# Optimization experiments

Hardware: AMD Instinct MI355X
Metric: run time of the kernel (lower is better)

The kernel has to match this reference:

```python
import jax, jax.numpy as jnp
import numpy as np

N_NODES = 100000
NEG_SLOPE = 0.01  # F.leaky_relu default


def _hetero_graphconv(x, src, dst, W, b, n_nodes):
    """HeteroGraphConv(aggregate='sum') of DGL GraphConv(norm='both') per edge type.

    x: [N, d_in]; src/dst: [R, E] int; W: [R, d_in, d_out]; b: [R, d_out].
    """
    n_rel = W.shape[0]
    ones = None
    out = jnp.zeros((n_nodes, W.shape[2]), dtype=x.dtype)
    for r in range(n_rel):  # small fixed number of relations
        s, d = src[r], dst[r]
        e_ones = jnp.ones(s.shape, dtype=x.dtype)
        deg_out = jnp.clip(jax.ops.segment_sum(e_ones, s, num_segments=n_nodes), 1.0)
        deg_in = jnp.clip(jax.ops.segment_sum(e_ones, d, num_segments=n_nodes), 1.0)
        # norm='both': scale src by out_deg^-1/2, aggregate, scale dst by in_deg^-1/2.
        # Apply weight before gather (aggregation is linear) to shrink edge traffic.
        h = (x * (deg_out ** -0.5)[:, None]) @ W[r]          # [N, d_out]
        agg = jax.ops.segment_sum(h[s], d, num_segments=n_nodes)  # gather-scatter over edges
        out = out + agg * (deg_in ** -0.5)[:, None] + b[r]
    return out


def setup_inputs() -> dict:
    key = jax.random.key(0)
    ks = jax.random.split(key, 8)
    d_in, d_h, d_out, n_cls, n_rel, n_edges = 256, 128, 128, 16, 3, 600000
    x = jax.random.normal(ks[0], (N_NODES, d_in), dtype=jnp.float32)
    src = jax.random.randint(ks[1], (n_rel, n_edges), 0, N_NODES, dtype=jnp.int32)
    dst = jax.random.randint(ks[2], (n_rel, n_edges), 0, N_NODES, dtype=jnp.int32)
    W0 = jax.random.normal(ks[3], (n_rel, d_in, d_h), dtype=jnp.float32) * (d_in ** -0.5)
    b0 = jnp.zeros((n_rel, d_h), dtype=jnp.float32)
    W1 = jax.random.normal(ks[4], (n_rel, d_h, d_out), dtype=jnp.float32) * (d_h ** -0.5)
    b1 = jnp.zeros((n_rel, d_out), dtype=jnp.float32)
    fc_W = jax.random.normal(ks[5], (d_out, n_cls), dtype=jnp.float32) * (d_out ** -0.5)
    fc_b = jnp.zeros((n_cls,), dtype=jnp.float32)
    return {"x": x, "src": src, "dst": dst, "W0": W0, "b0": b0,
            "W1": W1, "b1": b1, "fc_W": fc_W, "fc_b": fc_b}


def reference(x, src, dst, W0, b0, W1, b1, fc_W, fc_b):
    n = x.shape[0]
    h = _hetero_graphconv(x, src, dst, W0, b0, n)
    h = jax.nn.leaky_relu(h, negative_slope=NEG_SLOPE)  # dropout rate 0 (eval)
    h = _hetero_graphconv(h, src, dst, W1, b1, n)       # last layer: no activation
    logits = h @ fc_W + fc_b
    return (h, logits)
```

## Files before the change

### kernel.cpp

```cpp
#include <hip/hip_runtime.h>
#include <hip/hip_bf16.h>
#include <stdint.h>


typedef __attribute__((ext_vector_type(8))) short bf16x8;
typedef __attribute__((ext_vector_type(4))) float f32x4;
typedef unsigned short u16;

#define SCAN_T 256
#define SCAN_E 8
#define SCAN_BLK (SCAN_T * SCAN_E)

__global__ __launch_bounds__(256)
void hist_kernel(const int* __restrict__ src, const int* __restrict__ dst,
                 int* __restrict__ cnt_out8, int* __restrict__ cnt_in8,
                 int E, int N) {
    int e = blockIdx.x * blockDim.x + threadIdx.x;
    int r = blockIdx.y;
    if (e >= E) return;
    int copy = blockIdx.x & 7;
    size_t base = ((size_t)copy * 3 + r) * N;
    atomicAdd(cnt_out8 + base + src[(size_t)r * E + e], 1);
    atomicAdd(cnt_in8  + base + dst[(size_t)r * E + e], 1);
}

__global__ __launch_bounds__(256)
void reduce_scales_kernel(const int* __restrict__ cnt_out8, const int* __restrict__ cnt_in8,
                          float* __restrict__ s_out, float* __restrict__ s_in,
                          int* __restrict__ cnt_in, int total ) {
    int i = blockIdx.x * blockDim.x + threadIdx.x;
    if (i >= total) return;
    int co = 0, ci = 0;
#pragma unroll
    for (int c = 0; c < 8; c++) {
        co += cnt_out8[(size_t)c * total + i];
        ci += cnt_in8[(size_t)c * total + i];
    }
    s_out[i] = rsqrtf(fmaxf((float)co, 1.0f));
    s_in[i]  = rsqrtf(fmaxf((float)ci, 1.0f));
    cnt_in[i] = ci;
}

__global__ __launch_bounds__(SCAN_T)
void scan1_kernel(const int* __restrict__ cnt, int* __restrict__ pre,
                  int* __restrict__ bsums, int N) {
    int r = blockIdx.y, b = blockIdx.x, t = threadIdx.x;
    int base = b * SCAN_BLK + t * SCAN_E;
    int v[SCAN_E], s = 0;
#pragma unroll
    for (int j = 0; j < SCAN_E; j++) {
        int idx = base + j;
        v[j] = (idx < N) ? cnt[(size_t)r * N + idx] : 0;
        s += v[j];
    }
    __shared__ int sd[SCAN_T];
    sd[t] = s;
    __syncthreads();
    for (int off = 1; off < SCAN_T; off <<= 1) {
        int x = (t >= off) ? sd[t - off] : 0;
        __syncthreads();
        sd[t] += x;
        __syncthreads();
    }
    if (t == SCAN_T - 1) bsums[r * gridDim.x + b] = sd[t];
    int run = sd[t] - s;
#pragma unroll
    for (int j = 0; j < SCAN_E; j++) {
        int idx = base + j;
        if (idx < N) pre[(size_t)r * (N + 1) + idx] = run;
        run += v[j];
    }
}

__global__ void scan2_kernel(int* __restrict__ bsums, int* __restrict__ row_start,
                             int nb, int N) {
    for (int r = 0; r < 3; r++) {
        int run = 0;
        for (int b = 0; b < nb; b++) {
            int t = bsums[r * nb + b];
            bsums[r * nb + b] = run;
            run += t;
        }
        row_start[(size_t)r * (N + 1) + N] = run;
    }
}

__global__ __launch_bounds__(SCAN_T)
void scan3_kernel(int* __restrict__ pre, const int* __restrict__ bsums,
                  int* __restrict__ cursor, int nb, int N) {
    int r = blockIdx.y, b = blockIdx.x, t = threadIdx.x;
    int add = bsums[r * nb + b];
    int base = b * SCAN_BLK + t * SCAN_E;
#pragma unroll
    for (int j = 0; j < SCAN_E; j++) {
        int idx = base + j;
        if (idx < N) {
            int val = pre[(size_t)r * (N + 1) + idx] + add;
            pre[(size_t)r * (N + 1) + idx] = val;
            cursor[(size_t)r * N + idx] = val;
        }
    }
}

__global__ __launch_bounds__(256)
void bucket_fill_kernel(const int* __restrict__ src, const int* __restrict__ dst,
                        int* __restrict__ cursor, int* __restrict__ esrc,
                        int E, int N) {
    int e = blockIdx.x * blockDim.x + threadIdx.x;
    int r = blockIdx.y;
    if (e >= E) return;
    int d = dst[(size_t)r * E + e];
    int pos = atomicAdd(cursor + (size_t)r * N + d, 1);
    esrc[(size_t)r * E + pos] = src[(size_t)r * E + e];
}

__global__ __launch_bounds__(256)
void prep_w_kernel(const float* __restrict__ W0, const float* __restrict__ W1,
                   u16* __restrict__ w0hi, u16* __restrict__ w0lo,
                   u16* __restrict__ w1hi, u16* __restrict__ w1lo) {
    int idx = blockIdx.x * blockDim.x + threadIdx.x;
    const int n0 = 3 * 256 * 128;
    const int n1 = 3 * 128 * 128;
    if (idx >= n0 + n1) return;
    float f;
    u16 *phi, *plo;
    int oidx;
    if (idx < n0) {
        int r = idx / 32768, rem = idx % 32768;
        int n = rem / 256, k = rem % 256;
        f = W0[(size_t)r * 32768 + (size_t)k * 128 + n];
        phi = w0hi; plo = w0lo; oidx = idx;
    } else {
        int i2 = idx - n0;
        int r = i2 / 16384, rem = i2 % 16384;
        int n = rem / 128, k = rem % 128;
        f = W1[(size_t)r * 16384 + (size_t)k * 128 + n];
        phi = w1hi; plo = w1lo; oidx = i2;
    }
    uint32_t u = __float_as_uint(f);
    phi[oidx] = (u16)(u >> 16);
    float lo = f - __uint_as_float(u & 0xFFFF0000u);
    uint32_t ul = __float_as_uint(lo);
    plo[oidx] = (u16)((ul + 0x7FFFu + ((ul >> 16) & 1u)) >> 16);
}

__global__ __launch_bounds__(256)
void gemm_split_bf16(const float* __restrict__ A, const float* __restrict__ s_out,
                     const u16* __restrict__ Whi_all, const u16* __restrict__ Wlo_all,
                     u16* __restrict__ Cout_all, int M, int K, int Nn) {
    const int r = blockIdx.y;
    const float* scale = s_out + (size_t)r * Nn;
    const u16* Whi = Whi_all + (size_t)r * K * 128;
    const u16* Wlo = Wlo_all + (size_t)r * K * 128;
    u16* Cout = Cout_all + (size_t)r * Nn * 128;

    __shared__ u16 As_hi[128][40];
    __shared__ u16 As_lo[128][40];
    __shared__ u16 Bs_hi[128][40];
    __shared__ u16 Bs_lo[128][40];

    const int tid  = threadIdx.x;
    const int m0   = blockIdx.x * 128;
    const int lane = tid & 63;
    const int wave = tid >> 6;
    const int wm   = (wave & 1) * 64;
    const int wn   = (wave >> 1) * 64;
    const int lm   = lane & 15;
    const int kq   = (lane >> 4) * 8;

    f32x4 acc[4][4];
#pragma unroll
    for (int i = 0; i < 4; i++)
#pragma unroll
        for (int j = 0; j < 4; j++) acc[i][j] = (f32x4){0.f, 0.f, 0.f, 0.f};

    const int srow = tid >> 1;
    const int skb  = (tid & 1) * 16;

    const bool valid = (m0 + srow) < M;
    const float sval = valid ? scale[m0 + srow] : 0.f;
    const float* arow = A + (size_t)(m0 + srow) * K;
    const u16* whrow = Whi + (size_t)srow * K;
    const u16* wlrow = Wlo + (size_t)srow * K;

    for (int k0 = 0; k0 < K; k0 += 32) {
        float fa[16];
        if (valid) {
            *(float4*)&fa[0]  = *(const float4*)(arow + k0 + skb);
            *(float4*)&fa[4]  = *(const float4*)(arow + k0 + skb + 4);
            *(float4*)&fa[8]  = *(const float4*)(arow + k0 + skb + 8);
            *(float4*)&fa[12] = *(const float4*)(arow + k0 + skb + 12);
        } else {
#pragma unroll
            for (int i = 0; i < 16; i++) fa[i] = 0.f;
        }
        uint32_t ah[8], al[8];
#pragma unroll
        for (int p = 0; p < 8; p++) {
            float f0 = fa[2 * p] * sval, f1 = fa[2 * p + 1] * sval;
            uint32_t u0 = __float_as_uint(f0), u1 = __float_as_uint(f1);
            ah[p] = (u0 >> 16) | (u1 & 0xFFFF0000u);
            float l0 = f0 - __uint_as_float(u0 & 0xFFFF0000u);
            float l1 = f1 - __uint_as_float(u1 & 0xFFFF0000u);
            al[p] = (__float_as_uint(l0) >> 16) | (__float_as_uint(l1) & 0xFFFF0000u);
        }
        *(uint4*)&As_hi[srow][skb]     = *(uint4*)&ah[0];
        *(uint4*)&As_hi[srow][skb + 8] = *(uint4*)&ah[4];
        *(uint4*)&As_lo[srow][skb]     = *(uint4*)&al[0];
        *(uint4*)&As_lo[srow][skb + 8] = *(uint4*)&al[4];

        *(uint4*)&Bs_hi[srow][skb]     = *(const uint4*)(whrow + k0 + skb);
        *(uint4*)&Bs_hi[srow][skb + 8] = *(const uint4*)(whrow + k0 + skb + 8);
        *(uint4*)&Bs_lo[srow][skb]     = *(const uint4*)(wlrow + k0 + skb);
        *(uint4*)&Bs_lo[srow][skb + 8] = *(const uint4*)(wlrow + k0 + skb + 8);

        __syncthreads();

        bf16x8 a_hi[4], a_lo[4], b_hi[4], b_lo[4];
#pragma unroll
        for (int i = 0; i < 4; i++) {
            a_hi[i] = *(const bf16x8*)&As_hi[wm + i * 16 + lm][kq];
            a_lo[i] = *(const bf16x8*)&As_lo[wm + i * 16 + lm][kq];
            b_hi[i] = *(const bf16x8*)&Bs_hi[wn + i * 16 + lm][kq];
            b_lo[i] = *(const bf16x8*)&Bs_lo[wn + i * 16 + lm][kq];
        }
#pragma unroll
        for (int i = 0; i < 4; i++)
#pragma unroll
            for (int j = 0; j < 4; j++) {
                acc[i][j] = __builtin_amdgcn_mfma_f32_16x16x32_bf16(a_hi[i], b_hi[j], acc[i][j], 0, 0, 0);
                acc[i][j] = __builtin_amdgcn_mfma_f32_16x16x32_bf16(a_lo[i], b_hi[j], acc[i][j], 0, 0, 0);
                acc[i][j] = __builtin_amdgcn_mfma_f32_16x16x32_bf16(a_hi[i], b_lo[j], acc[i][j], 0, 0, 0);
            }
        __syncthreads();
    }

    const int rq = (lane >> 4) * 4;
#pragma unroll
    for (int i = 0; i < 4; i++) {
        int mbase = m0 + wm + i * 16 + rq;
#pragma unroll
        for (int j = 0; j < 4; j++) {
            int col = wn + j * 16 + lm;
#pragma unroll
            for (int rg = 0; rg < 4; rg++) {
                int m = mbase + rg;
                if (m < M) {
                    uint32_t u = __float_as_uint(acc[i][j][rg]);
                    Cout[(size_t)m * 128 + col] =
                        (u16)((u + 0x7FFFu + ((u >> 16) & 1u)) >> 16);
                }
            }
        }
    }
}

#define BF16_LO(u) __uint_as_float((u) << 16)
#define BF16_HI(u) __uint_as_float((u) & 0xFFFF0000u)

__device__ __forceinline__ void gather_rel(const uint32_t* __restrict__ h,
                                           const int* __restrict__ es,
                                           int beg, int end,
                                           float& ox, float& oy, float w) {
    float ax = 0.f, ay = 0.f, cx = 0.f, cy = 0.f;
    int e = beg;
    for (; e + 4 <= end; e += 4) {
        int s0 = es[e], s1 = es[e + 1], s2 = es[e + 2], s3 = es[e + 3];
        uint32_t u0 = h[(size_t)s0 * 64];
        uint32_t u1 = h[(size_t)s1 * 64];
        uint32_t u2 = h[(size_t)s2 * 64];
        uint32_t u3 = h[(size_t)s3 * 64];
        ax += BF16_LO(u0); ay += BF16_HI(u0);
        cx += BF16_LO(u1); cy += BF16_HI(u1);
        ax += BF16_LO(u2); ay += BF16_HI(u2);
        cx += BF16_LO(u3); cy += BF16_HI(u3);
    }
    if (e + 2 <= end) {
        int s0 = es[e], s1 = es[e + 1];
        uint32_t u0 = h[(size_t)s0 * 64];
        uint32_t u1 = h[(size_t)s1 * 64];
        ax += BF16_LO(u0); ay += BF16_HI(u0);
        cx += BF16_LO(u1); cy += BF16_HI(u1);
        e += 2;
    }
    if (e < end) {
        uint32_t u0 = h[(size_t)es[e] * 64];
        ax += BF16_LO(u0); ay += BF16_HI(u0);
    }
    ox += (ax + cx) * w;
    oy += (ay + cy) * w;
}

__global__ __launch_bounds__(256)
void gather_l0(const u16* __restrict__ hb, const int* __restrict__ row_start,
               const int* __restrict__ esrc, const float* __restrict__ s_in,
               const float* __restrict__ b, float* __restrict__ out, int N, int E) {
    int node = blockIdx.x * 4 + (threadIdx.x >> 6);
    if (node >= N) return;
    int lane = threadIdx.x & 63;
    float tx = 0.f, ty = 0.f;
#pragma unroll
    for (int r = 0; r < 3; r++) {
        const int* rs = row_start + (size_t)r * (N + 1);
        gather_rel((const uint32_t*)hb + (size_t)r * N * 64 + lane,
                   esrc + (size_t)r * E, rs[node], rs[node + 1],
                   tx, ty, s_in[(size_t)r * N + node]);
    }
    int c0 = lane * 2;
    tx += b[c0] + b[128 + c0] + b[256 + c0];
    ty += b[c0 + 1] + b[128 + c0 + 1] + b[256 + c0 + 1];
    tx = fmaxf(tx, 0.f) + 0.01f * fminf(tx, 0.f);
    ty = fmaxf(ty, 0.f) + 0.01f * fminf(ty, 0.f);
    *(float2*)(out + (size_t)node * 128 + c0) = make_float2(tx, ty);
}

__global__ __launch_bounds__(256)
void gather_l1(const u16* __restrict__ hb, const int* __restrict__ row_start,
               const int* __restrict__ esrc, const float* __restrict__ s_in,
               const float* __restrict__ b, const float* __restrict__ fcW,
               const float* __restrict__ fcb, float* __restrict__ out_h,
               float* __restrict__ out_logits, int N, int E) {
    int node = blockIdx.x * 4 + (threadIdx.x >> 6);
    if (node >= N) return;
    int lane = threadIdx.x & 63;
    float tx = 0.f, ty = 0.f;
#pragma unroll
    for (int r = 0; r < 3; r++) {
        const int* rs = row_start + (size_t)r * (N + 1);
        gather_rel((const uint32_t*)hb + (size_t)r * N * 64 + lane,
                   esrc + (size_t)r * E, rs[node], rs[node + 1],
                   tx, ty, s_in[(size_t)r * N + node]);
    }
    int c0 = lane * 2;
    tx += b[c0] + b[128 + c0] + b[256 + c0];
    ty += b[c0 + 1] + b[128 + c0 + 1] + b[256 + c0 + 1];
    *(float2*)(out_h + (size_t)node * 128 + c0) = make_float2(tx, ty);

    const float* fc0 = fcW + (size_t)c0 * 16;
    float p[16];
#pragma unroll
    for (int j = 0; j < 16; j++) p[j] = tx * fc0[j] + ty * fc0[16 + j];
#pragma unroll
    for (int off = 1; off < 64; off <<= 1) {
#pragma unroll
        for (int j = 0; j < 16; j++) p[j] += __shfl_xor(p[j], off);
    }
    if (lane == 0) {
        float* lp = out_logits + (size_t)node * 16;
        *(float4*)(lp + 0)  = make_float4(p[0] + fcb[0],  p[1] + fcb[1],  p[2] + fcb[2],  p[3] + fcb[3]);
        *(float4*)(lp + 4)  = make_float4(p[4] + fcb[4],  p[5] + fcb[5],  p[6] + fcb[6],  p[7] + fcb[7]);
        *(float4*)(lp + 8)  = make_float4(p[8] + fcb[8],  p[9] + fcb[9],  p[10] + fcb[10], p[11] + fcb[11]);
        *(float4*)(lp + 12) = make_float4(p[12] + fcb[12], p[13] + fcb[13], p[14] + fcb[14], p[15] + fcb[15]);
    }
}

extern "C" void kernel_launch(void* const* d_in, const int* in_sizes, int n_in,
                              void* d_out, int out_size, void* d_ws, size_t ws_size,
                              hipStream_t stream) {
    const float* x   = (const float*)d_in[0];
    const int*   src = (const int*)d_in[1];
    const int*   dst = (const int*)d_in[2];
    const float* W0  = (const float*)d_in[3];
    const float* b0  = (const float*)d_in[4];
    const float* W1  = (const float*)d_in[5];
    const float* b1  = (const float*)d_in[6];
    const float* fcW = (const float*)d_in[7];
    const float* fcb = (const float*)d_in[8];

    const int N = in_sizes[0] / 256;
    const int E = in_sizes[1] / 3;
    const int nb = (N + SCAN_BLK - 1) / SCAN_BLK;

    float* out_h      = (float*)d_out;
    float* out_logits = out_h + (size_t)N * 128;

    char* p = (char*)d_ws;
    auto alloc = [&](size_t bytes) -> char* {
        char* q = p;
        p += (bytes + 255) & ~(size_t)255;
        return q;
    };
    float* s_out     = (float*)alloc(3 * (size_t)N * 4);
    float* s_in      = (float*)alloc(3 * (size_t)N * 4);
    int*   cnt8      = (int*)alloc(2 * 8 * 3 * (size_t)N * 4);
    int*   cnt_out8  = cnt8;
    int*   cnt_in8   = cnt8 + 8 * 3 * (size_t)N;
    int*   cnt_in    = (int*)alloc(3 * (size_t)N * 4);
    int*   row_start = (int*)alloc(3 * (size_t)(N + 1) * 4);
    int*   cursor    = (int*)alloc(3 * (size_t)N * 4);
    int*   bsums     = (int*)alloc(1024 * 4);
    int*   esrc      = (int*)alloc(3 * (size_t)E * 4);
    u16*   w0hi      = (u16*)alloc(3 * 256 * 128 * 2);
    u16*   w0lo      = (u16*)alloc(3 * 256 * 128 * 2);
    u16*   w1hi      = (u16*)alloc(3 * 128 * 128 * 2);
    u16*   w1lo      = (u16*)alloc(3 * 128 * 128 * 2);
    u16*   hb        = (u16*)alloc(3 * (size_t)N * 128 * 2);
    float* acc0      = (float*)alloc((size_t)N * 128 * 4);

    hipMemsetAsync(cnt8, 0, 2 * 8 * 3 * (size_t)N * sizeof(int), stream);

    hist_kernel<<<dim3((E + 255) / 256, 3), 256, 0, stream>>>(src, dst, cnt_out8, cnt_in8, E, N);
    reduce_scales_kernel<<<(3 * N + 255) / 256, 256, 0, stream>>>(
        cnt_out8, cnt_in8, s_out, s_in, cnt_in, 3 * N);

    scan1_kernel<<<dim3(nb, 3), SCAN_T, 0, stream>>>(cnt_in, row_start, bsums, N);
    scan2_kernel<<<1, 1, 0, stream>>>(bsums, row_start, nb, N);
    scan3_kernel<<<dim3(nb, 3), SCAN_T, 0, stream>>>(row_start, bsums, cursor, nb, N);
    bucket_fill_kernel<<<dim3((E + 255) / 256, 3), 256, 0, stream>>>(src, dst, cursor, esrc, E, N);

    prep_w_kernel<<<(3 * 256 * 128 + 3 * 128 * 128 + 255) / 256, 256, 0, stream>>>(
        W0, W1, w0hi, w0lo, w1hi, w1lo);

    int gemm_blocks   = (N + 127) / 128;
    int gather_blocks = (N + 3) / 4;

    gemm_split_bf16<<<dim3(gemm_blocks, 3), 256, 0, stream>>>(
        x, s_out, w0hi, w0lo, hb, N, 256, N);
    gather_l0<<<gather_blocks, 256, 0, stream>>>(hb, row_start, esrc, s_in, b0, acc0, N, E);

    gemm_split_bf16<<<dim3(gemm_blocks, 3), 256, 0, stream>>>(
        acc0, s_out, w1hi, w1lo, hb, N, 128, N);
    gather_l1<<<gather_blocks, 256, 0, stream>>>(hb, row_start, esrc, s_in, b1, fcW, fcb,
                                                 out_h, out_logits, N, E);
}
```

Before: 846.3 us.

## Gather edges with 16-byte loads across four edge groups per wave

The gather kernels change from one 4-byte load per lane per edge to a layout where each wave splits into 4 groups of 16 lanes. Each lane loads a uint4 (8 bf16 channels), so four edges are processed in parallel, and the groups are reduced with shuffles. The fc logits reduction is restructured to match, cutting the shuffle work from 16 values over 6 steps to 4 values over 4 steps. The GEMM now applies the per-row src-degree scale in the epilogue instead of on the A input, which changes rounding slightly. Loop iterations past the end of a node's edges are masked, adding some wasted loads when degrees are small.

```diff
diff --git a/kernel.cpp b/kernel.cpp
--- a/kernel.cpp
+++ b/kernel.cpp
@@ -178,7 +178,6 @@
     const int skb  = (tid & 1) * 16;
 
     const bool valid = (m0 + srow) < M;
-    const float sval = valid ? scale[m0 + srow] : 0.f;
     const float* arow = A + (size_t)(m0 + srow) * K;
     const u16* whrow = Whi + (size_t)srow * K;
     const u16* wlrow = Wlo + (size_t)srow * K;
@@ -197,7 +196,7 @@
         uint32_t ah[8], al[8];
 #pragma unroll
         for (int p = 0; p < 8; p++) {
-            float f0 = fa[2 * p] * sval, f1 = fa[2 * p + 1] * sval;
+            float f0 = fa[2 * p], f1 = fa[2 * p + 1];
             uint32_t u0 = __float_as_uint(f0), u1 = __float_as_uint(f1);
             ah[p] = (u0 >> 16) | (u1 & 0xFFFF0000u);
             float l0 = f0 - __uint_as_float(u0 & 0xFFFF0000u);
@@ -240,13 +239,14 @@
     for (int i = 0; i < 4; i++) {
         int mbase = m0 + wm + i * 16 + rq;
 #pragma unroll
-        for (int j = 0; j < 4; j++) {
-            int col = wn + j * 16 + lm;
-#pragma unroll
-            for (int rg = 0; rg < 4; rg++) {
-                int m = mbase + rg;
-                if (m < M) {
-                    uint32_t u = __float_as_uint(acc[i][j][rg]);
+        for (int rg = 0; rg < 4; rg++) {
+            int m = mbase + rg;
+            if (m < M) {
+                float s = scale[m];
+#pragma unroll
+                for (int j = 0; j < 4; j++) {
+                    int col = wn + j * 16 + lm;
+                    uint32_t u = __float_as_uint(acc[i][j][rg] * s);
                     Cout[(size_t)m * 128 + col] =
                         (u16)((u + 0x7FFFu + ((u >> 16) & 1u)) >> 16);
                 }
@@ -258,37 +258,51 @@
 #define BF16_LO(u) __uint_as_float((u) << 16)
 #define BF16_HI(u) __uint_as_float((u) & 0xFFFF0000u)
 
-__device__ __forceinline__ void gather_rel(const uint32_t* __restrict__ h,
-                                           const int* __restrict__ es,
-                                           int beg, int end,
-                                           float& ox, float& oy, float w) {
-    float ax = 0.f, ay = 0.f, cx = 0.f, cy = 0.f;
-    int e = beg;
-    for (; e + 4 <= end; e += 4) {
-        int s0 = es[e], s1 = es[e + 1], s2 = es[e + 2], s3 = es[e + 3];
-        uint32_t u0 = h[(size_t)s0 * 64];
-        uint32_t u1 = h[(size_t)s1 * 64];
-        uint32_t u2 = h[(size_t)s2 * 64];
-        uint32_t u3 = h[(size_t)s3 * 64];
-        ax += BF16_LO(u0); ay += BF16_HI(u0);
-        cx += BF16_LO(u1); cy += BF16_HI(u1);
-        ax += BF16_LO(u2); ay += BF16_HI(u2);
-        cx += BF16_LO(u3); cy += BF16_HI(u3);
-    }
-    if (e + 2 <= end) {
-        int s0 = es[e], s1 = es[e + 1];
-        uint32_t u0 = h[(size_t)s0 * 64];
-        uint32_t u1 = h[(size_t)s1 * 64];
-        ax += BF16_LO(u0); ay += BF16_HI(u0);
-        cx += BF16_LO(u1); cy += BF16_HI(u1);
-        e += 2;
-    }
-    if (e < end) {
-        uint32_t u0 = h[(size_t)es[e] * 64];
-        ax += BF16_LO(u0); ay += BF16_HI(u0);
-    }
-    ox += (ax + cx) * w;
-    oy += (ay + cy) * w;
+#define ADD8(a, u)                                   \
+    do {                                             \
+        a[0] += BF16_LO((u).x); a[1] += BF16_HI((u).x); \
+        a[2] += BF16_LO((u).y); a[3] += BF16_HI((u).y); \
+        a[4] += BF16_LO((u).z); a[5] += BF16_HI((u).z); \
+        a[6] += BF16_LO((u).w); a[7] += BF16_HI((u).w); \
+    } while (0)
+
+__device__ __forceinline__ void gather3(const u16* __restrict__ hb,
+                                        const int* __restrict__ row_start,
+                                        const int* __restrict__ esrc,
+                                        const float* __restrict__ s_in,
+                                        int node, int g, int c, int N, int E,
+                                        float* __restrict__ tot ) {
+    const uint4* hbase = (const uint4*)hb;
+#pragma unroll
+    for (int r = 0; r < 3; r++) {
+        const int* rs = row_start + (size_t)r * (N + 1);
+        const int* es = esrc + (size_t)r * E;
+        const uint4* h = hbase + (size_t)r * N * 16 + c;
+        int beg = rs[node], end = rs[node + 1];
+        float a[8];
+#pragma unroll
+        for (int j = 0; j < 8; j++) a[j] = 0.f;
+        for (int e = beg; e < end; e += 8) {
+            int e0 = e + g, e1 = e + 4 + g;
+            bool v0 = e0 < end, v1 = e1 < end;
+            int i0 = es[v0 ? e0 : beg];
+            int i1 = es[v1 ? e1 : beg];
+            uint4 u0 = h[(size_t)i0 * 16];
+            uint4 u1 = h[(size_t)i1 * 16];
+            if (!v0) u0 = make_uint4(0u, 0u, 0u, 0u);
+            if (!v1) u1 = make_uint4(0u, 0u, 0u, 0u);
+            ADD8(a, u0);
+            ADD8(a, u1);
+        }
+        float w = s_in[(size_t)r * N + node];
+#pragma unroll
+        for (int j = 0; j < 8; j++) tot[j] += a[j] * w;
+    }
+#pragma unroll
+    for (int j = 0; j < 8; j++) {
+        tot[j] += __shfl_xor(tot[j], 16);
+        tot[j] += __shfl_xor(tot[j], 32);
+    }
 }
 
 __global__ __launch_bounds__(256)
@@ -298,20 +312,21 @@
     int node = blockIdx.x * 4 + (threadIdx.x >> 6);
     if (node >= N) return;
     int lane = threadIdx.x & 63;
-    float tx = 0.f, ty = 0.f;
-#pragma unroll
-    for (int r = 0; r < 3; r++) {
-        const int* rs = row_start + (size_t)r * (N + 1);
-        gather_rel((const uint32_t*)hb + (size_t)r * N * 64 + lane,
-                   esrc + (size_t)r * E, rs[node], rs[node + 1],
-                   tx, ty, s_in[(size_t)r * N + node]);
-    }
-    int c0 = lane * 2;
-    tx += b[c0] + b[128 + c0] + b[256 + c0];
-    ty += b[c0 + 1] + b[128 + c0 + 1] + b[256 + c0 + 1];
-    tx = fmaxf(tx, 0.f) + 0.01f * fminf(tx, 0.f);
-    ty = fmaxf(ty, 0.f) + 0.01f * fminf(ty, 0.f);
-    *(float2*)(out + (size_t)node * 128 + c0) = make_float2(tx, ty);
+    int g = lane >> 4, c = lane & 15;
+    float tot[8];
+#pragma unroll
+    for (int j = 0; j < 8; j++) tot[j] = 0.f;
+    gather3(hb, row_start, esrc, s_in, node, g, c, N, E, tot);
+    int cb = c * 8;
+#pragma unroll
+    for (int j = 0; j < 8; j++) {
+        float v = tot[j] + b[cb + j] + b[128 + cb + j] + b[256 + cb + j];
+        tot[j] = fmaxf(v, 0.f) + 0.01f * fminf(v, 0.f);
+    }
+    if (g == 0)
+        *(float4*)(out + (size_t)node * 128 + cb) = make_float4(tot[0], tot[1], tot[2], tot[3]);
+    else if (g == 1)
+        *(float4*)(out + (size_t)node * 128 + cb + 4) = make_float4(tot[4], tot[5], tot[6], tot[7]);
 }
 
 __global__ __launch_bounds__(256)
@@ -323,34 +338,40 @@
     int node = blockIdx.x * 4 + (threadIdx.x >> 6);
     if (node >= N) return;
     int lane = threadIdx.x & 63;
-    float tx = 0.f, ty = 0.f;
-#pragma unroll
-    for (int r = 0; r < 3; r++) {
-        const int* rs = row_start + (size_t)r * (N + 1);
-        gather_rel((const uint32_t*)hb + (size_t)r * N * 64 + lane,
-                   esrc + (size_t)r * E, rs[node], rs[node + 1],
-                   tx, ty, s_in[(size_t)r * N + node]);
-    }
-    int c0 = lane * 2;
-    tx += b[c0] + b[128 + c0] + b[256 + c0];
-    ty += b[c0 + 1] + b[128 + c0 + 1] + b[256 + c0 + 1];
-    *(float2*)(out_h + (size_t)node * 128 + c0) = make_float2(tx, ty);
-
-    const float* fc0 = fcW + (size_t)c0 * 16;
-    float p[16];
-#pragma unroll
-    for (int j = 0; j < 16; j++) p[j] = tx * fc0[j] + ty * fc0[16 + j];
-#pragma unroll
-    for (int off = 1; off < 64; off <<= 1) {
-#pragma unroll
-        for (int j = 0; j < 16; j++) p[j] += __shfl_xor(p[j], off);
-    }
-    if (lane == 0) {
-        float* lp = out_logits + (size_t)node * 16;
-        *(float4*)(lp + 0)  = make_float4(p[0] + fcb[0],  p[1] + fcb[1],  p[2] + fcb[2],  p[3] + fcb[3]);
-        *(float4*)(lp + 4)  = make_float4(p[4] + fcb[4],  p[5] + fcb[5],  p[6] + fcb[6],  p[7] + fcb[7]);
-        *(float4*)(lp + 8)  = make_float4(p[8] + fcb[8],  p[9] + fcb[9],  p[10] + fcb[10], p[11] + fcb[11]);
-        *(float4*)(lp + 12) = make_float4(p[12] + fcb[12], p[13] + fcb[13], p[14] + fcb[14], p[15] + fcb[15]);
+    int g = lane >> 4, c = lane & 15;
+    float tot[8];
+#pragma unroll
+    for (int j = 0; j < 8; j++) tot[j] = 0.f;
+    gather3(hb, row_start, esrc, s_in, node, g, c, N, E, tot);
+    int cb = c * 8;
+#pragma unroll
+    for (int j = 0; j < 8; j++)
+        tot[j] += b[cb + j] + b[128 + cb + j] + b[256 + cb + j];
+    if (g == 0)
+        *(float4*)(out_h + (size_t)node * 128 + cb) = make_float4(tot[0], tot[1], tot[2], tot[3]);
+    else if (g == 1)
+        *(float4*)(out_h + (size_t)node * 128 + cb + 4) = make_float4(tot[4], tot[5], tot[6], tot[7]);
+
+    float p0 = 0.f, p1 = 0.f, p2 = 0.f, p3 = 0.f;
+#pragma unroll
+    for (int j = 0; j < 8; j++) {
+        const float* fw = fcW + (size_t)(cb + j) * 16 + g * 4;
+        p0 += tot[j] * fw[0];
+        p1 += tot[j] * fw[1];
+        p2 += tot[j] * fw[2];
+        p3 += tot[j] * fw[3];
+    }
+#pragma unroll
+    for (int off = 1; off < 16; off <<= 1) {
+        p0 += __shfl_xor(p0, off);
+        p1 += __shfl_xor(p1, off);
+        p2 += __shfl_xor(p2, off);
+        p3 += __shfl_xor(p3, off);
+    }
+    if (c == 0) {
+        int jb = g * 4;
+        *(float4*)(out_logits + (size_t)node * 16 + jb) =
+            make_float4(p0 + fcb[jb], p1 + fcb[jb + 1], p2 + fcb[jb + 2], p3 + fcb[jb + 3]);
     }
 }
 
```

Result: slower. 865.9 us (+2.3%).
